# Optimization experiments

Measured on AMD Instinct MI355X. Metric: run time of the kernel, lower is better.

## Reference

```python
import jax, jax.numpy as jnp
import numpy as np

N = 50000      # nodes
E = 800000     # edges
IN = 128       # input features (arxiv)
HID = 128      # hidden per head
HEADS = 3      # arxiv_data=True -> 3 heads
OUT = 40       # classes
EPS = 1e-5     # BN eps
SLOPE = 0.2    # DGL GATConv leaky_relu negative slope


def setup_inputs() -> dict:
    key = jax.random.key(0)
    ks = jax.random.split(key, 20)
    x = jax.random.normal(ks[0], (N, IN), jnp.float32)
    src = jax.random.randint(ks[1], (E,), 0, N, dtype=jnp.int32)
    # guarantee every node has >=1 in-edge so edge_softmax is well-defined
    dst = jnp.concatenate([jnp.arange(N, dtype=jnp.int32),
                           jax.random.randint(ks[2], (E - N,), 0, N, dtype=jnp.int32)])

    def lin(k, fi, fo):
        return jax.random.normal(k, (fi, fo), jnp.float32) * (1.0 / np.sqrt(fi))

    def attn(k, h, d):
        return jax.random.normal(k, (h, d), jnp.float32) * 0.1

    return {
        "x": x, "src": src, "dst": dst,
        # layer 0: IN -> HEADS*HID
        "W0": lin(ks[3], IN, HEADS * HID),
        "al0": attn(ks[4], HEADS, HID), "ar0": attn(ks[5], HEADS, HID),
        "b0": jnp.zeros((HEADS * HID,), jnp.float32),
        # layer 1: HEADS*HID -> HEADS*HID
        "W1": lin(ks[6], HEADS * HID, HEADS * HID),
        "al1": attn(ks[7], HEADS, HID), "ar1": attn(ks[8], HEADS, HID),
        "b1": jnp.zeros((HEADS * HID,), jnp.float32),
        # layer 2: HEADS*HID -> OUT, 1 head
        "W2": lin(ks[9], HEADS * HID, OUT),
        "al2": attn(ks[10], 1, OUT), "ar2": attn(ks[11], 1, OUT),
        "b2": jnp.zeros((OUT,), jnp.float32),
        # batch norms over HEADS*HID channels
        "g0": jnp.ones((HEADS * HID,), jnp.float32), "be0": jnp.zeros((HEADS * HID,), jnp.float32),
        "g1": jnp.ones((HEADS * HID,), jnp.float32), "be1": jnp.zeros((HEADS * HID,), jnp.float32),
    }


def gat_layer(h, src, dst, W, al, ar, b, heads, d_out):
    # fc + per-head split: [N, heads, d_out]
    f = (h @ W).reshape(-1, heads, d_out)
    el = jnp.einsum('nhd,hd->nh', f, al)          # [N, H]
    er = jnp.einsum('nhd,hd->nh', f, ar)          # [N, H]
    e = jax.nn.leaky_relu(el[src] + er[dst], SLOPE)  # [E, H]
    # edge softmax over incoming edges of each dst node
    m = jax.ops.segment_max(e, dst, num_segments=N)
    ex = jnp.exp(e - m[dst])
    s = jax.ops.segment_sum(ex, dst, num_segments=N)
    a = ex / s[dst]                                # [E, H]
    # u_mul_e + sum aggregation
    out = jax.ops.segment_sum(f[src] * a[:, :, None], dst, num_segments=N)  # [N, H, D]
    out = out + b.reshape(1, heads, d_out)
    return out.reshape(-1, heads * d_out)


def batch_norm(h, g, b):
    mu = h.mean(axis=0)
    var = h.var(axis=0)
    return g * (h - mu) / jnp.sqrt(var + EPS) + b


def reference(x, src, dst, W0, al0, ar0, b0, W1, al1, ar1, b1,
              W2, al2, ar2, b2, g0, be0, g1, be1):
    h = gat_layer(x, src, dst, W0, al0, ar0, b0, HEADS, HID)
    h = jax.nn.relu(batch_norm(h, g0, be0))        # dropout: eval mode (identity)
    h = gat_layer(h, src, dst, W1, al1, ar1, b1, HEADS, HID)
    h = jax.nn.relu(batch_norm(h, g1, be1))
    out = gat_layer(h, src, dst, W2, al2, ar2, b2, 1, OUT)
    return out
```

## Files before the change

kernel.cpp:

```cpp
#include <hip/hip_runtime.h>
#include <hip/hip_bf16.h>

typedef __hip_bfloat16 bf16;
typedef __attribute__((ext_vector_type(8))) short short8;
typedef __attribute__((ext_vector_type(4))) float f32x4;

static constexpr int N_NODES  = 50000;
static constexpr int N_EDGES  = 800000;
static constexpr int F_IN     = 128;
static constexpr int D_HID    = 128;
static constexpr int H_HEADS  = 3;
static constexpr int F_OUT    = 40;
static constexpr float BN_EPS = 1e-5f;
static constexpr float SLOPE  = 0.2f;

__device__ __forceinline__ float bfLo(unsigned int u) { return __uint_as_float(u << 16); }
__device__ __forceinline__ float bfHi(unsigned int u) { return __uint_as_float(u & 0xffff0000u); }
__device__ __forceinline__ float bfs(unsigned short s) { return __uint_as_float(((unsigned int)s) << 16); }
__device__ __forceinline__ unsigned int packbf(float a, float b) {
  union { bf16 h[2]; unsigned int u; } pk;
  pk.h[0] = __float2bfloat16(a);
  pk.h[1] = __float2bfloat16(b);
  return pk.u;
}
__device__ __forceinline__ short f2bf_s(float v) {
  bf16 h = __float2bfloat16(v);
  union { bf16 b; short s; } c; c.b = h; return c.s;
}

__global__ __launch_bounds__(256) void gemm_mfma(const short* __restrict__ A,
                                                 const short* __restrict__ WT,
                                                 bf16* __restrict__ C,
                                                 const float* __restrict__ alp,
                                                 const float* __restrict__ arp,
                                                 float* __restrict__ el,
                                                 float* __restrict__ er,
                                                 const float* __restrict__ scale,
                                                 const float* __restrict__ shift,
                                                 int M, int K, int Nc, int els, int ers,
                                                 int lda, int adiag) {
  constexpr int BM = 128, BN = 128, BK = 64, LDP = BK + 8;
  __shared__ short As[BM * LDP];
  __shared__ short Bs[BN * LDP];
  __shared__ float ecomb[128][4];
  int tid = threadIdx.x;
  int wave = tid >> 6, lane = tid & 63;
  int bm = blockIdx.y, bn = blockIdx.x;
  int m15 = lane & 15, quad = lane >> 4;
  int ksub = quad * 8;
  int wr = wave >> 1, wc = wave & 1;
  int srow = tid >> 3;
  int scol = (tid & 7) * 8;
  int acol0 = adiag ? bn * K : 0;

  f32x4 acc[4][4];
#pragma unroll
  for (int i = 0; i < 4; ++i)
#pragma unroll
    for (int j = 0; j < 4; ++j) acc[i][j] = (f32x4){0.f, 0.f, 0.f, 0.f};

  for (int k0 = 0; k0 < K; k0 += BK) {
    int cb = acol0 + k0 + scol;
    f32x4 sc0, sc1, sh0, sh1;
    if (scale) {
      sc0 = *(const f32x4*)&scale[cb]; sc1 = *(const f32x4*)&scale[cb + 4];
      sh0 = *(const f32x4*)&shift[cb]; sh1 = *(const f32x4*)&shift[cb + 4];
    }
#pragma unroll
    for (int c = 0; c < 4; ++c) {
      int r = srow + c * 32;
      int gr = bm * BM + r; if (gr >= M) gr = M - 1;
      short8 av = *(const short8*)&A[(size_t)gr * lda + acol0 + k0 + scol];
      if (scale) {
#pragma unroll
        for (int j = 0; j < 8; ++j) {
          float v = bfs((unsigned short)av[j]);
          float s = (j < 4) ? ((const float*)&sc0)[j] : ((const float*)&sc1)[j - 4];
          float t = (j < 4) ? ((const float*)&sh0)[j] : ((const float*)&sh1)[j - 4];
          float y = v * s + t;
          av[j] = f2bf_s(y > 0.f ? y : 0.f);
        }
      }
      *(short8*)&As[r * LDP + scol] = av;
      int gn = bn * BN + r;
      *(short8*)&Bs[r * LDP + scol] = *(const short8*)&WT[(size_t)gn * K + k0 + scol];
    }
    __syncthreads();
#pragma unroll
    for (int ks = 0; ks < BK; ks += 32) {
      short8 a[4], b[4];
#pragma unroll
      for (int i = 0; i < 4; ++i)
        a[i] = *(const short8*)&As[(wr * 64 + i * 16 + m15) * LDP + ks + ksub];
#pragma unroll
      for (int j = 0; j < 4; ++j)
        b[j] = *(const short8*)&Bs[(wc * 64 + j * 16 + m15) * LDP + ks + ksub];
#pragma unroll
      for (int i = 0; i < 4; ++i)
#pragma unroll
        for (int j = 0; j < 4; ++j)
          acc[i][j] = __builtin_amdgcn_mfma_f32_16x16x32_bf16(a[i], b[j], acc[i][j], 0, 0, 0);
    }
    __syncthreads();
  }

  int h = bn;
  float alv[4], arv[4];
#pragma unroll
  for (int j = 0; j < 4; ++j) {
    int col = bn * BN + wc * 64 + j * 16 + m15;
    alv[j] = alp[col];
    arv[j] = arp[col];
  }
#pragma unroll
  for (int i = 0; i < 4; ++i) {
#pragma unroll
    for (int r = 0; r < 4; ++r) {
      int rl = wr * 64 + i * 16 + quad * 4 + r;
      int row = bm * BM + rl;
      float pe = 0.f, pr = 0.f;
#pragma unroll
      for (int j = 0; j < 4; ++j) {
        float v = acc[i][j][r];
        pe += v * alv[j];
        pr += v * arv[j];
        int col = bn * BN + wc * 64 + j * 16 + m15;
        if (row < M && col < Nc)
          C[(size_t)row * Nc + col] = __float2bfloat16(v);
      }
#pragma unroll
      for (int off = 1; off < 16; off <<= 1) {
        pe += __shfl_xor(pe, off);
        pr += __shfl_xor(pr, off);
      }
      if (m15 == 0) {
        ecomb[rl][wc] = pe;
        ecomb[rl][2 + wc] = pr;
      }
    }
  }
  __syncthreads();
  if (tid < 128) {
    int row = bm * BM + tid;
    if (row < M) {
      el[(size_t)row * els + h] = ecomb[tid][0] + ecomb[tid][1];
      er[(size_t)row * ers + h] = ecomb[tid][2] + ecomb[tid][3];
    }
  }
}

__global__ void prep_kernel(const float* __restrict__ x, bf16* __restrict__ abuf,
                            const float* __restrict__ W0, const float* __restrict__ W1,
                            const float* __restrict__ W2, bf16* __restrict__ WT0,
                            bf16* __restrict__ WT1, bf16* __restrict__ WT2,
                            const float* __restrict__ al2, const float* __restrict__ ar2,
                            float* __restrict__ alp2, float* __restrict__ arp2,
                            int* __restrict__ cnt) {
  const int NTOT = N_NODES * F_IN;
  for (int i = blockIdx.x * blockDim.x + threadIdx.x; i < NTOT;
       i += gridDim.x * blockDim.x) {
    abuf[i] = __float2bfloat16(x[i]);
    if (i < 384 * 384) { int n = i / 384, k = i - n * 384; WT1[i] = __float2bfloat16(W1[(size_t)k * 384 + n]); }
    if (i < 384 * 128) { int n = i / 128, k = i - n * 128; WT0[i] = __float2bfloat16(W0[(size_t)k * 384 + n]); }
    if (i < 128 * 384) { int n = i / 384, k = i - n * 384; WT2[i] = __float2bfloat16(n < F_OUT ? W2[(size_t)k * F_OUT + n] : 0.f); }
    if (i < 2 * N_NODES) cnt[i] = 0;
    if (i < 128) { alp2[i] = i < F_OUT ? al2[i] : 0.f; arp2[i] = i < F_OUT ? ar2[i] : 0.f; }
  }
}

__global__ __launch_bounds__(256) void vlr_kernel(const float* __restrict__ W0,
                                                  const float* __restrict__ al0,
                                                  const float* __restrict__ ar0,
                                                  float* __restrict__ vl,
                                                  float* __restrict__ vr) {
  int wid = (blockIdx.x * 256 + threadIdx.x) >> 6;
  int lane = threadIdx.x & 63;
  int h = wid >> 7, k = wid & 127;
  const float2* wrow = (const float2*)(W0 + (size_t)k * 384 + h * 128);
  const float2* av = (const float2*)(al0 + h * 128);
  const float2* rv = (const float2*)(ar0 + h * 128);
  float2 wv = wrow[lane], a2 = av[lane], r2 = rv[lane];
  float sl = wv.x * a2.x + wv.y * a2.y;
  float sr = wv.x * r2.x + wv.y * r2.y;
#pragma unroll
  for (int off = 32; off > 0; off >>= 1) {
    sl += __shfl_xor(sl, off);
    sr += __shfl_xor(sr, off);
  }
  if (lane == 0) { vl[wid] = sl; vr[wid] = sr; }
}

__global__ __launch_bounds__(256) void elr_kernel(const unsigned int* __restrict__ x2,
                                                  const float* __restrict__ vl,
                                                  const float* __restrict__ vr,
                                                  float* __restrict__ el,
                                                  float* __restrict__ er, int N) {
  int wv = threadIdx.x >> 6, lane = threadIdx.x & 63;
  int n = blockIdx.x * 4 + wv;
  if (n >= N) return;
  unsigned int u = x2[(size_t)n * 64 + lane];
  float v0 = bfLo(u), v1 = bfHi(u);
  float pl[3], pr[3];
#pragma unroll
  for (int h = 0; h < 3; ++h) {
    float2 a2 = *(const float2*)&vl[h * 128 + 2 * lane];
    float2 r2 = *(const float2*)&vr[h * 128 + 2 * lane];
    pl[h] = v0 * a2.x + v1 * a2.y;
    pr[h] = v0 * r2.x + v1 * r2.y;
  }
#pragma unroll
  for (int h = 0; h < 3; ++h) {
#pragma unroll
    for (int off = 32; off > 0; off >>= 1) {
      pl[h] += __shfl_xor(pl[h], off);
      pr[h] += __shfl_xor(pr[h], off);
    }
  }
  if (lane == 0) {
    *(float4*)&el[(size_t)n * 4] = make_float4(pl[0], pl[1], pl[2], 0.f);
    er[(size_t)n * 3 + 0] = pr[0];
    er[(size_t)n * 3 + 1] = pr[1];
    er[(size_t)n * 3 + 2] = pr[2];
  }
}

__global__ void hist_kernel(const int* __restrict__ dst, int* __restrict__ cnt, int E) {
  int i = blockIdx.x * blockDim.x + threadIdx.x;
  if (i < E) atomicAdd(cnt + dst[i], 1);
}

__global__ void scan_part_kernel(const int* __restrict__ cnt, int* __restrict__ blksum, int N) {
  __shared__ int sh[256];
  int i = blockIdx.x * 256 + threadIdx.x;
  sh[threadIdx.x] = (i < N) ? cnt[i] : 0;
  __syncthreads();
  for (int off = 128; off > 0; off >>= 1) {
    if (threadIdx.x < off) sh[threadIdx.x] += sh[threadIdx.x + off];
    __syncthreads();
  }
  if (threadIdx.x == 0) blksum[blockIdx.x] = sh[0];
}

__global__ void scan_write_kernel(const int* __restrict__ cnt, const int* __restrict__ blksum,
                                  int* __restrict__ row_ptr, int N, int E, int nblk) {
  __shared__ int top[256];
  __shared__ int sh[256];
  int t = threadIdx.x;
  int vt = (t < nblk) ? blksum[t] : 0;
  top[t] = vt;
  __syncthreads();
  for (int off = 1; off < 256; off <<= 1) {
    int u = (t >= off) ? top[t - off] : 0;
    __syncthreads();
    top[t] += u;
    __syncthreads();
  }
  int blkoff = (blockIdx.x == 0) ? 0 : top[blockIdx.x - 1];
  int i = blockIdx.x * 256 + t;
  int v = (i < N) ? cnt[i] : 0;
  sh[t] = v;
  __syncthreads();
  for (int off = 1; off < 256; off <<= 1) {
    int u = (t >= off) ? sh[t - off] : 0;
    __syncthreads();
    sh[t] += u;
    __syncthreads();
  }
  if (i < N) row_ptr[i] = blkoff + sh[t] - v;
  if (i == 0) row_ptr[N] = E;
}

__global__ void scatter_kernel(const int* __restrict__ src, const int* __restrict__ dst,
                               const int* __restrict__ row_ptr, int* __restrict__ fill,
                               int* __restrict__ csr_src, int E) {
  int i = blockIdx.x * blockDim.x + threadIdx.x;
  if (i < E) {
    int d = dst[i];
    int pos = row_ptr[d] + atomicAdd(fill + d, 1);
    csr_src[pos] = src[i];
  }
}

__global__ __launch_bounds__(256) void aggr_x_kernel(
    const int* __restrict__ row_ptr, const int* __restrict__ csr_src,
    const float4* __restrict__ el4, const float* __restrict__ er,
    const uint4* __restrict__ xq, uint4* __restrict__ outq,
    float* __restrict__ bnzero, int N) {
  if (blockIdx.x == 0) {
    for (int j = threadIdx.x; j < 2 * H_HEADS * D_HID; j += 256) bnzero[j] = 0.f;
  }
  __shared__ float wls[4][64 * 3];
  __shared__ int   sls[4][64];
  int wv = threadIdx.x >> 6;
  int d = (blockIdx.x * 256 + threadIdx.x) >> 6;
  int lane = threadIdx.x & 63;
  if (d >= N) return;
  int beg = row_ptr[d], end = row_ptr[d + 1];
  float* mywls = wls[wv];
  int* mysls = sls[wv];
  int g = lane >> 4;
  int cch = lane & 15;

  float erd[3];
#pragma unroll
  for (int h = 0; h < 3; ++h) erd[h] = er[d * 3 + h];
  float acc[3][8];
#pragma unroll
  for (int h = 0; h < 3; ++h)
#pragma unroll
    for (int j = 0; j < 8; ++j) acc[h][j] = 0.f;
  float sp[3] = {0.f, 0.f, 0.f};

  for (int k0 = beg; k0 < end; k0 += 64) {
    int nk = end - k0; if (nk > 64) nk = 64;
    if (lane < nk) {
      int s_l = csr_src[k0 + lane];
      mysls[lane] = s_l;
      float4 e4 = el4[s_l];
      float ev[3] = {e4.x, e4.y, e4.z};
#pragma unroll
      for (int h = 0; h < 3; ++h) {
        float sc = ev[h] + erd[h];
        sc = sc > 0.f ? sc : SLOPE * sc;
        float w = __expf(sc);
        mywls[lane * 3 + h] = w;
        sp[h] += w;
      }
    }
    for (int e0 = 0; e0 < nk; e0 += 4) {
      int e = e0 + g;
      if (e < nk) {
        int se = mysls[e];
        float w0s = mywls[e * 3], w1s = mywls[e * 3 + 1], w2s = mywls[e * 3 + 2];
        uint4 u = xq[(size_t)se * 16 + cch];
        float ff[8] = {bfLo(u.x), bfHi(u.x), bfLo(u.y), bfHi(u.y),
                       bfLo(u.z), bfHi(u.z), bfLo(u.w), bfHi(u.w)};
#pragma unroll
        for (int j = 0; j < 8; ++j) {
          acc[0][j] += w0s * ff[j];
          acc[1][j] += w1s * ff[j];
          acc[2][j] += w2s * ff[j];
        }
      }
    }
  }
#pragma unroll
  for (int h = 0; h < 3; ++h) {
#pragma unroll
    for (int off = 32; off > 0; off >>= 1) sp[h] += __shfl_xor(sp[h], off);
  }
#pragma unroll
  for (int h = 0; h < 3; ++h)
#pragma unroll
    for (int j = 0; j < 8; ++j) {
      acc[h][j] += __shfl_xor(acc[h][j], 16);
      acc[h][j] += __shfl_xor(acc[h][j], 32);
    }
  if (g < 3) {
    float og[8];
#pragma unroll
    for (int j = 0; j < 8; ++j)
      og[j] = (g == 0) ? acc[0][j] : (g == 1) ? acc[1][j] : acc[2][j];
    float spg = (g == 0) ? sp[0] : (g == 1) ? sp[1] : sp[2];
    float inv = 1.f / spg;
    uint4 r;
    r.x = packbf(og[0] * inv, og[1] * inv);
    r.y = packbf(og[2] * inv, og[3] * inv);
    r.z = packbf(og[4] * inv, og[5] * inv);
    r.w = packbf(og[6] * inv, og[7] * inv);
    outq[(size_t)d * 48 + g * 16 + cch] = r;
  }
}

template <int H, int D>
__global__ __launch_bounds__(256) void aggr_fused_kernel(
    const int* __restrict__ row_ptr, const int* __restrict__ csr_src,
    const float4* __restrict__ el4, const float* __restrict__ er,
    const bf16* __restrict__ f, uint4* __restrict__ outq,
    float* __restrict__ bnzero, int N) {
  if (blockIdx.x == 0) {
    for (int j = threadIdx.x; j < 2 * H * D; j += 256) bnzero[j] = 0.f;
  }
  constexpr int W = H * D / 2;
  constexpr int WQ = W / 4;
  __shared__ float wls[4][64 * H];
  int wv = threadIdx.x >> 6;
  int d = (blockIdx.x * 256 + threadIdx.x) >> 6;
  int lane = threadIdx.x & 63;
  if (d >= N) return;
  int beg = row_ptr[d], end = row_ptr[d + 1];
  const uint4* fq = (const uint4*)f;
  float* mywls = wls[wv];
  int hsel = lane >> 4;

  float erd[H];
#pragma unroll
  for (int h = 0; h < H; ++h) erd[h] = er[d * H + h];
  float acc[8];
#pragma unroll
  for (int j = 0; j < 8; ++j) acc[j] = 0.f;
  float sp[H];
#pragma unroll
  for (int h = 0; h < H; ++h) sp[h] = 0.f;

  for (int k0 = beg; k0 < end; k0 += 64) {
    int nk = end - k0; if (nk > 64) nk = 64;
    int s_l = 0;
    if (lane < nk) {
      s_l = csr_src[k0 + lane];
      float4 e4 = el4[s_l];
      float ev[3] = {e4.x, e4.y, e4.z};
#pragma unroll
      for (int h = 0; h < H; ++h) {
        float sc = ev[h] + erd[h];
        sc = sc > 0.f ? sc : SLOPE * sc;
        float w = __expf(sc);
        mywls[lane * H + h] = w;
        sp[h] += w;
      }
    }
    for (int e = 0; e < nk; ++e) {
      int se = __shfl(s_l, e);
      if (lane < WQ) {
        float w = mywls[e * H + hsel];
        uint4 u = fq[(size_t)se * WQ + lane];
        acc[0] += w * bfLo(u.x); acc[1] += w * bfHi(u.x);
        acc[2] += w * bfLo(u.y); acc[3] += w * bfHi(u.y);
        acc[4] += w * bfLo(u.z); acc[5] += w * bfHi(u.z);
        acc[6] += w * bfLo(u.w); acc[7] += w * bfHi(u.w);
      }
    }
  }
#pragma unroll
  for (int h = 0; h < H; ++h) {
#pragma unroll
    for (int off = 32; off > 0; off >>= 1) sp[h] += __shfl_xor(sp[h], off);
  }
  if (lane < WQ) {
    float inv = 1.f / sp[hsel];
    uint4 r;
    r.x = packbf(acc[0] * inv, acc[1] * inv);
    r.y = packbf(acc[2] * inv, acc[3] * inv);
    r.z = packbf(acc[4] * inv, acc[5] * inv);
    r.w = packbf(acc[6] * inv, acc[7] * inv);
    outq[(size_t)d * WQ + lane] = r;
  }
}

__global__ __launch_bounds__(256) void aggr_out_kernel(
    const int* __restrict__ row_ptr, const int* __restrict__ csr_src,
    const float* __restrict__ el, const float* __restrict__ er,
    const bf16* __restrict__ f, const float* __restrict__ bias,
    float* __restrict__ out, int N) {
  constexpr int DW = F_OUT / 2;
  __shared__ float wls[4][64];
  __shared__ int   sls[4][64];
  int wv = threadIdx.x >> 6;
  int d = (blockIdx.x * 256 + threadIdx.x) >> 6;
  int lane = threadIdx.x & 63;
  if (d >= N) return;
  int beg = row_ptr[d], end = row_ptr[d + 1];
  const unsigned int* fu = (const unsigned int*)f;
  float* mywls = wls[wv];
  int* mysls = sls[wv];
  int g = lane / DW;
  int cch = lane - g * DW;
  float erd = er[d];
  float a0 = 0.f, a1 = 0.f, sp = 0.f;
  for (int k0 = beg; k0 < end; k0 += 64) {
    int nk = end - k0; if (nk > 64) nk = 64;
    if (lane < nk) {
      int s_l = csr_src[k0 + lane];
      mysls[lane] = s_l;
      float sc = el[s_l] + erd;
      sc = sc > 0.f ? sc : SLOPE * sc;
      float w = __expf(sc);
      mywls[lane] = w;
      sp += w;
    }
    for (int e0 = 0; e0 < nk; e0 += 3) {
      int e = e0 + g;
      if (g < 3 && e < nk) {
        int se = mysls[e];
        float w = mywls[e];
        unsigned int u = fu[(size_t)se * DW + cch];
        a0 += w * bfLo(u);
        a1 += w * bfHi(u);
      }
    }
  }
#pragma unroll
  for (int off = 32; off > 0; off >>= 1) sp += __shfl_xor(sp, off);
  float b0 = __shfl(a0, (lane + DW) & 63), b1 = __shfl(a1, (lane + DW) & 63);
  float c0 = __shfl(a0, (lane + 2 * DW) & 63), c1 = __shfl(a1, (lane + 2 * DW) & 63);
  if (lane < DW) {
    float inv = 1.f / sp;
    float o0 = (a0 + b0 + c0) * inv + bias[2 * lane];
    float o1 = (a1 + b1 + c1) * inv + bias[2 * lane + 1];
    *(float2*)&out[(size_t)d * F_OUT + 2 * lane] = make_float2(o0, o1);
  }
}

__global__ void bn_stats_kernel(const unsigned int* __restrict__ h2, float* __restrict__ sum,
                                float* __restrict__ sumsq, int N, int C2) {
  int c = threadIdx.x;
  int step = gridDim.x;
  float s0 = 0.f, q0 = 0.f, s1 = 0.f, q1 = 0.f;
  int n = blockIdx.x;
  for (; n + 3 * step < N; n += 4 * step) {
    unsigned int ua = h2[(size_t)n * C2 + c];
    unsigned int ub = h2[(size_t)(n + step) * C2 + c];
    unsigned int uc = h2[(size_t)(n + 2 * step) * C2 + c];
    unsigned int ud = h2[(size_t)(n + 3 * step) * C2 + c];
    float va0 = bfLo(ua), va1 = bfHi(ua);
    float vb0 = bfLo(ub), vb1 = bfHi(ub);
    float vc0 = bfLo(uc), vc1 = bfHi(uc);
    float vd0 = bfLo(ud), vd1 = bfHi(ud);
    s0 += va0 + vb0 + vc0 + vd0;
    s1 += va1 + vb1 + vc1 + vd1;
    q0 += va0 * va0 + vb0 * vb0 + vc0 * vc0 + vd0 * vd0;
    q1 += va1 * va1 + vb1 * vb1 + vc1 * vc1 + vd1 * vd1;
  }
  for (; n < N; n += step) {
    unsigned int u = h2[(size_t)n * C2 + c];
    float v0 = bfLo(u), v1 = bfHi(u);
    s0 += v0; q0 += v0 * v0;
    s1 += v1; q1 += v1 * v1;
  }
  atomicAdd(sum + 2 * c, s0);
  atomicAdd(sum + 2 * c + 1, s1);
  atomicAdd(sumsq + 2 * c, q0);
  atomicAdd(sumsq + 2 * c + 1, q1);
}

__global__ void bn_finalize_kernel(const float* __restrict__ sum, const float* __restrict__ sumsq,
                                   const float* __restrict__ g, const float* __restrict__ be,
                                   float* __restrict__ scale, float* __restrict__ shift,
                                   int N, int C) {
  int c = threadIdx.x;
  if (c >= C) return;
  float inv_n = 1.f / (float)N;
  float mu = sum[c] * inv_n;
  float var = sumsq[c] * inv_n - mu * mu;
  float sc = g[c] * rsqrtf(var + BN_EPS);
  scale[c] = sc;
  shift[c] = be[c] - mu * sc;
}

static inline int cdiv(int a, int b) { return (a + b - 1) / b; }

extern "C" void kernel_launch(void* const* d_in, const int* in_sizes, int n_in,
                              void* d_out, int out_size, void* d_ws, size_t ws_size,
                              hipStream_t stream) {
  const float* x   = (const float*)d_in[0];
  const int* src   = (const int*)d_in[1];
  const int* dst   = (const int*)d_in[2];
  const float* W0  = (const float*)d_in[3];
  const float* al0 = (const float*)d_in[4];
  const float* ar0 = (const float*)d_in[5];
  const float* W1  = (const float*)d_in[7];
  const float* al1 = (const float*)d_in[8];
  const float* ar1 = (const float*)d_in[9];
  const float* W2  = (const float*)d_in[11];
  const float* al2 = (const float*)d_in[12];
  const float* ar2 = (const float*)d_in[13];
  const float* b2  = (const float*)d_in[14];
  const float* g0  = (const float*)d_in[15];
  const float* be0 = (const float*)d_in[16];
  const float* g1  = (const float*)d_in[17];
  const float* be1 = (const float*)d_in[18];
  float* out = (float*)d_out;

  const int N = N_NODES, E = N_EDGES, H = H_HEADS;
  const int C = H * D_HID;
  const int nblk = cdiv(N, 256);

  char* p = (char*)d_ws;
  auto take = [&](size_t bytes) {
    char* r = p;
    p += (bytes + 255) & ~(size_t)255;
    return r;
  };
  bf16*   f_buf   = (bf16*) take((size_t)N * C * sizeof(bf16));
  bf16*   hbuf    = (bf16*) take((size_t)N * C * sizeof(bf16));
  bf16*   abuf    = (bf16*) take((size_t)N * C * sizeof(bf16));
  float*  elbuf   = (float*)take((size_t)N * 4 * sizeof(float));
  float*  er      = (float*)take((size_t)N * H * sizeof(float));
  float*  bnbuf   = (float*)take((size_t)2 * C * sizeof(float));
  float*  scbuf   = (float*)take((size_t)2 * C * sizeof(float));
  bf16*   WT0     = (bf16*) take((size_t)C * F_IN * sizeof(bf16));
  bf16*   WT1     = (bf16*) take((size_t)C * C * sizeof(bf16));
  bf16*   WT2     = (bf16*) take((size_t)128 * C * sizeof(bf16));
  float*  alp2    = (float*)take(128 * sizeof(float));
  float*  arp2    = (float*)take(128 * sizeof(float));
  float*  vlbuf   = (float*)take(384 * sizeof(float));
  float*  vrbuf   = (float*)take(384 * sizeof(float));
  int*    cnt     = (int*)take((size_t)2 * N * sizeof(int));
  int*    row_ptr = (int*)take((size_t)(N + 1) * sizeof(int));
  int*    csr_src = (int*)take((size_t)E * sizeof(int));
  int*    blksum  = (int*)take(256 * sizeof(int));
  float*  bnsum = bnbuf, *bnsq = bnbuf + C;
  float*  scv = scbuf, *shv = scbuf + C;
  int*    fill  = cnt + N;

  prep_kernel<<<cdiv(N * F_IN, 256), 256, 0, stream>>>(x, abuf, W0, W1, W2, WT0, WT1, WT2,
                                                       al2, ar2, alp2, arp2, cnt);
  vlr_kernel<<<96, 256, 0, stream>>>(W0, al0, ar0, vlbuf, vrbuf);
  elr_kernel<<<cdiv(N, 4), 256, 0, stream>>>((const unsigned int*)abuf, vlbuf, vrbuf,
                                             elbuf, er, N);
  hist_kernel<<<cdiv(E, 256), 256, 0, stream>>>(dst, cnt, E);
  scan_part_kernel<<<nblk, 256, 0, stream>>>(cnt, blksum, N);
  scan_write_kernel<<<nblk, 256, 0, stream>>>(cnt, blksum, row_ptr, N, E, nblk);
  scatter_kernel<<<cdiv(E, 256), 256, 0, stream>>>(src, dst, row_ptr, fill, csr_src, E);

  aggr_x_kernel<<<cdiv(N * 64, 256), 256, 0, stream>>>(
      row_ptr, csr_src, (const float4*)elbuf, er, (const uint4*)abuf,
      (uint4*)f_buf, bnbuf, N);
  gemm_mfma<<<dim3(3, cdiv(N, 128)), 256, 0, stream>>>(
      (const short*)f_buf, (const short*)WT0, hbuf, al0, ar0, elbuf, er,
      nullptr, nullptr, N, F_IN, C, 4, 3, C, 1);
  bn_stats_kernel<<<1024, C / 2, 0, stream>>>((const unsigned int*)hbuf, bnsum, bnsq, N, C / 2);
  bn_finalize_kernel<<<1, C, 0, stream>>>(bnsum, bnsq, g0, be0, scv, shv, N, C);

  gemm_mfma<<<dim3(C / 128, cdiv(N, 128)), 256, 0, stream>>>(
      (const short*)hbuf, (const short*)WT1, f_buf, al1, ar1, elbuf, er,
      scv, shv, N, C, C, 4, 3, C, 0);
  aggr_fused_kernel<H_HEADS, D_HID><<<cdiv(N * 64, 256), 256, 0, stream>>>(
      row_ptr, csr_src, (const float4*)elbuf, er, f_buf, (uint4*)hbuf, bnbuf, N);
  bn_stats_kernel<<<1024, C / 2, 0, stream>>>((const unsigned int*)hbuf, bnsum, bnsq, N, C / 2);
  bn_finalize_kernel<<<1, C, 0, stream>>>(bnsum, bnsq, g1, be1, scv, shv, N, C);

  gemm_mfma<<<dim3(1, cdiv(N, 128)), 256, 0, stream>>>(
      (const short*)hbuf, (const short*)WT2, f_buf, alp2, arp2, elbuf, er,
      scv, shv, N, C, F_OUT, 1, 1, C, 0);
  aggr_out_kernel<<<cdiv(N * 64, 256), 256, 0, stream>>>(
      row_ptr, csr_src, elbuf, er, f_buf, b2, out, N);
}
```

Measured before the change: 598.7 us.

## Process four edges per wavefront iteration in fused GAT aggregation

Restructures the per-node aggregation so each 16-lane group handles a different edge, with each lane loading three 16-byte chunks (one per head), instead of only 48 of 64 lanes working on one edge at a time. Partial sums are combined across the four lane groups with cross-lane shuffles at the end. The aim is to use all lanes, keep more loads in flight and cut the serial edge loop length by four. The cost is more accumulator registers (24 floats) and an extra cross-lane reduction per node. The head count is now hardcoded to 3 instead of following the template parameter.

```diff
diff --git a/kernel.cpp b/kernel.cpp
--- a/kernel.cpp
+++ b/kernel.cpp
@@ -381,9 +381,9 @@
   if (blockIdx.x == 0) {
     for (int j = threadIdx.x; j < 2 * H * D; j += 256) bnzero[j] = 0.f;
   }
-  constexpr int W = H * D / 2;
-  constexpr int WQ = W / 4;
-  __shared__ float wls[4][64 * H];
+  constexpr int WQ = H * D / 8;
+  __shared__ float wls[4][64 * 3];
+  __shared__ int   sls[4][64];
   int wv = threadIdx.x >> 6;
   int d = (blockIdx.x * 256 + threadIdx.x) >> 6;
   int lane = threadIdx.x & 63;
@@ -391,59 +391,85 @@
   int beg = row_ptr[d], end = row_ptr[d + 1];
   const uint4* fq = (const uint4*)f;
   float* mywls = wls[wv];
-  int hsel = lane >> 4;
-
-  float erd[H];
-#pragma unroll
-  for (int h = 0; h < H; ++h) erd[h] = er[d * H + h];
-  float acc[8];
-#pragma unroll
-  for (int j = 0; j < 8; ++j) acc[j] = 0.f;
-  float sp[H];
-#pragma unroll
-  for (int h = 0; h < H; ++h) sp[h] = 0.f;
+  int* mysls = sls[wv];
+  int g = lane >> 4;
+  int cch = lane & 15;
+
+  float erd[3];
+#pragma unroll
+  for (int h = 0; h < 3; ++h) erd[h] = er[d * 3 + h];
+  float acc[3][8];
+#pragma unroll
+  for (int p = 0; p < 3; ++p)
+#pragma unroll
+    for (int j = 0; j < 8; ++j) acc[p][j] = 0.f;
+  float sp[3] = {0.f, 0.f, 0.f};
 
   for (int k0 = beg; k0 < end; k0 += 64) {
     int nk = end - k0; if (nk > 64) nk = 64;
-    int s_l = 0;
     if (lane < nk) {
-      s_l = csr_src[k0 + lane];
+      int s_l = csr_src[k0 + lane];
+      mysls[lane] = s_l;
       float4 e4 = el4[s_l];
       float ev[3] = {e4.x, e4.y, e4.z};
 #pragma unroll
-      for (int h = 0; h < H; ++h) {
+      for (int h = 0; h < 3; ++h) {
         float sc = ev[h] + erd[h];
         sc = sc > 0.f ? sc : SLOPE * sc;
         float w = __expf(sc);
-        mywls[lane * H + h] = w;
+        mywls[lane * 3 + h] = w;
         sp[h] += w;
       }
     }
-    for (int e = 0; e < nk; ++e) {
-      int se = __shfl(s_l, e);
-      if (lane < WQ) {
-        float w = mywls[e * H + hsel];
-        uint4 u = fq[(size_t)se * WQ + lane];
-        acc[0] += w * bfLo(u.x); acc[1] += w * bfHi(u.x);
-        acc[2] += w * bfLo(u.y); acc[3] += w * bfHi(u.y);
-        acc[4] += w * bfLo(u.z); acc[5] += w * bfHi(u.z);
-        acc[6] += w * bfLo(u.w); acc[7] += w * bfHi(u.w);
-      }
-    }
-  }
-#pragma unroll
-  for (int h = 0; h < H; ++h) {
+    for (int e0 = 0; e0 < nk; e0 += 4) {
+      int e = e0 + g;
+      if (e < nk) {
+        int se = mysls[e];
+        float w0s = mywls[e * 3], w1s = mywls[e * 3 + 1], w2s = mywls[e * 3 + 2];
+        const uint4* rp = &fq[(size_t)se * WQ + cch];
+        uint4 u0 = rp[0];
+        uint4 u1 = rp[16];
+        uint4 u2 = rp[32];
+        acc[0][0] += w0s * bfLo(u0.x); acc[0][1] += w0s * bfHi(u0.x);
+        acc[0][2] += w0s * bfLo(u0.y); acc[0][3] += w0s * bfHi(u0.y);
+        acc[0][4] += w0s * bfLo(u0.z); acc[0][5] += w0s * bfHi(u0.z);
+        acc[0][6] += w0s * bfLo(u0.w); acc[0][7] += w0s * bfHi(u0.w);
+        acc[1][0] += w1s * bfLo(u1.x); acc[1][1] += w1s * bfHi(u1.x);
+        acc[1][2] += w1s * bfLo(u1.y); acc[1][3] += w1s * bfHi(u1.y);
+        acc[1][4] += w1s * bfLo(u1.z); acc[1][5] += w1s * bfHi(u1.z);
+        acc[1][6] += w1s * bfLo(u1.w); acc[1][7] += w1s * bfHi(u1.w);
+        acc[2][0] += w2s * bfLo(u2.x); acc[2][1] += w2s * bfHi(u2.x);
+        acc[2][2] += w2s * bfLo(u2.y); acc[2][3] += w2s * bfHi(u2.y);
+        acc[2][4] += w2s * bfLo(u2.z); acc[2][5] += w2s * bfHi(u2.z);
+        acc[2][6] += w2s * bfLo(u2.w); acc[2][7] += w2s * bfHi(u2.w);
+      }
+    }
+  }
+#pragma unroll
+  for (int h = 0; h < 3; ++h) {
 #pragma unroll
     for (int off = 32; off > 0; off >>= 1) sp[h] += __shfl_xor(sp[h], off);
   }
-  if (lane < WQ) {
-    float inv = 1.f / sp[hsel];
+#pragma unroll
+  for (int p = 0; p < 3; ++p)
+#pragma unroll
+    for (int j = 0; j < 8; ++j) {
+      acc[p][j] += __shfl_xor(acc[p][j], 16);
+      acc[p][j] += __shfl_xor(acc[p][j], 32);
+    }
+  if (g < 3) {
+    float og[8];
+#pragma unroll
+    for (int j = 0; j < 8; ++j)
+      og[j] = (g == 0) ? acc[0][j] : (g == 1) ? acc[1][j] : acc[2][j];
+    float spg = (g == 0) ? sp[0] : (g == 1) ? sp[1] : sp[2];
+    float inv = 1.f / spg;
     uint4 r;
-    r.x = packbf(acc[0] * inv, acc[1] * inv);
-    r.y = packbf(acc[2] * inv, acc[3] * inv);
-    r.z = packbf(acc[4] * inv, acc[5] * inv);
-    r.w = packbf(acc[6] * inv, acc[7] * inv);
-    outq[(size_t)d * WQ + lane] = r;
+    r.x = packbf(og[0] * inv, og[1] * inv);
+    r.y = packbf(og[2] * inv, og[3] * inv);
+    r.z = packbf(og[4] * inv, og[5] * inv);
+    r.w = packbf(og[6] * inv, og[7] * inv);
+    outq[(size_t)d * WQ + g * 16 + cch] = r;
   }
 }
 
```

Measured after the change: 606.4 us. Within noise of the previous version (+1.3%).

## Fuse BN stats into layer-0 GEMM epilogue and merge small setup kernels

Applied to the files above, without the earlier changes.

Layer-0 batch-norm sum and sum-of-squares are now accumulated in the GEMM epilogue with per-column atomics, which removes one bn_stats pass over hbuf. The vl/vr projection is folded into prep_kernel and the dst histogram into elr_kernel, cutting two launches. The final GEMM output now uses a padded 64-column row stride for better-aligned gathers in aggr_out. The changes add atomic contention on BN columns and give float sums a nondeterministic order. They also assume bnbuf is zero, since the bn_stats kernel that presumably reset it no longer runs for layer 0.

```diff
diff --git a/kernel.cpp b/kernel.cpp
--- a/kernel.cpp
+++ b/kernel.cpp
@@ -37,8 +37,9 @@
                                                  float* __restrict__ er,
                                                  const float* __restrict__ scale,
                                                  const float* __restrict__ shift,
+                                                 float* __restrict__ bnstats,
                                                  int M, int K, int Nc, int els, int ers,
-                                                 int lda, int adiag) {
+                                                 int lda, int ldc, int adiag) {
   constexpr int BM = 128, BN = 128, BK = 64, LDP = BK + 8;
   __shared__ short As[BM * LDP];
   __shared__ short Bs[BN * LDP];
@@ -112,6 +113,7 @@
     alv[j] = alp[col];
     arv[j] = arp[col];
   }
+  float csum[4] = {0.f, 0.f, 0.f, 0.f}, csq[4] = {0.f, 0.f, 0.f, 0.f};
 #pragma unroll
   for (int i = 0; i < 4; ++i) {
 #pragma unroll
@@ -124,9 +126,10 @@
         float v = acc[i][j][r];
         pe += v * alv[j];
         pr += v * arv[j];
+        if (bnstats && row < M) { csum[j] += v; csq[j] += v * v; }
         int col = bn * BN + wc * 64 + j * 16 + m15;
         if (row < M && col < Nc)
-          C[(size_t)row * Nc + col] = __float2bfloat16(v);
+          C[(size_t)row * ldc + col] = __float2bfloat16(v);
       }
 #pragma unroll
       for (int off = 1; off < 16; off <<= 1) {
@@ -136,6 +139,21 @@
       if (m15 == 0) {
         ecomb[rl][wc] = pe;
         ecomb[rl][2 + wc] = pr;
+      }
+    }
+  }
+  if (bnstats) {
+#pragma unroll
+    for (int j = 0; j < 4; ++j) {
+      csum[j] += __shfl_xor(csum[j], 16); csum[j] += __shfl_xor(csum[j], 32);
+      csq[j]  += __shfl_xor(csq[j], 16);  csq[j]  += __shfl_xor(csq[j], 32);
+    }
+    if (quad == 0) {
+#pragma unroll
+      for (int j = 0; j < 4; ++j) {
+        int col = bn * BN + wc * 64 + j * 16 + m15;
+        atomicAdd(bnstats + col, csum[j]);
+        atomicAdd(bnstats + Nc + col, csq[j]);
       }
     }
   }
@@ -155,7 +173,9 @@
                             bf16* __restrict__ WT1, bf16* __restrict__ WT2,
                             const float* __restrict__ al2, const float* __restrict__ ar2,
                             float* __restrict__ alp2, float* __restrict__ arp2,
-                            int* __restrict__ cnt) {
+                            int* __restrict__ cnt,
+                            const float* __restrict__ al0, const float* __restrict__ ar0,
+                            float* __restrict__ vl, float* __restrict__ vr) {
   const int NTOT = N_NODES * F_IN;
   for (int i = blockIdx.x * blockDim.x + threadIdx.x; i < NTOT;
        i += gridDim.x * blockDim.x) {
@@ -166,35 +186,35 @@
     if (i < 2 * N_NODES) cnt[i] = 0;
     if (i < 128) { alp2[i] = i < F_OUT ? al2[i] : 0.f; arp2[i] = i < F_OUT ? ar2[i] : 0.f; }
   }
-}
-
-__global__ __launch_bounds__(256) void vlr_kernel(const float* __restrict__ W0,
-                                                  const float* __restrict__ al0,
-                                                  const float* __restrict__ ar0,
-                                                  float* __restrict__ vl,
-                                                  float* __restrict__ vr) {
-  int wid = (blockIdx.x * 256 + threadIdx.x) >> 6;
-  int lane = threadIdx.x & 63;
-  int h = wid >> 7, k = wid & 127;
-  const float2* wrow = (const float2*)(W0 + (size_t)k * 384 + h * 128);
-  const float2* av = (const float2*)(al0 + h * 128);
-  const float2* rv = (const float2*)(ar0 + h * 128);
-  float2 wv = wrow[lane], a2 = av[lane], r2 = rv[lane];
-  float sl = wv.x * a2.x + wv.y * a2.y;
-  float sr = wv.x * r2.x + wv.y * r2.y;
-#pragma unroll
-  for (int off = 32; off > 0; off >>= 1) {
-    sl += __shfl_xor(sl, off);
-    sr += __shfl_xor(sr, off);
-  }
-  if (lane == 0) { vl[wid] = sl; vr[wid] = sr; }
+  if (blockIdx.x < 96) {
+    int wid = blockIdx.x * 4 + (threadIdx.x >> 6);
+    int lane = threadIdx.x & 63;
+    int h = wid >> 7, k = wid & 127;
+    const float2* wrow = (const float2*)(W0 + (size_t)k * 384 + h * 128);
+    const float2* av = (const float2*)(al0 + h * 128);
+    const float2* rv = (const float2*)(ar0 + h * 128);
+    float2 wv = wrow[lane], a2 = av[lane], r2 = rv[lane];
+    float sl = wv.x * a2.x + wv.y * a2.y;
+    float sr = wv.x * r2.x + wv.y * r2.y;
+#pragma unroll
+    for (int off = 32; off > 0; off >>= 1) {
+      sl += __shfl_xor(sl, off);
+      sr += __shfl_xor(sr, off);
+    }
+    if (lane == 0) { vl[wid] = sl; vr[wid] = sr; }
+  }
 }
 
 __global__ __launch_bounds__(256) void elr_kernel(const unsigned int* __restrict__ x2,
                                                   const float* __restrict__ vl,
                                                   const float* __restrict__ vr,
                                                   float* __restrict__ el,
-                                                  float* __restrict__ er, int N) {
+                                                  float* __restrict__ er,
+                                                  const int* __restrict__ dst,
+                                                  int* __restrict__ cnt,
+                                                  int N, int E) {
+  int gid = blockIdx.x * 256 + threadIdx.x;
+  if (gid < E) atomicAdd(cnt + dst[gid], 1);
   int wv = threadIdx.x >> 6, lane = threadIdx.x & 63;
   int n = blockIdx.x * 4 + wv;
   if (n >= N) return;
@@ -222,11 +242,6 @@
     er[(size_t)n * 3 + 1] = pr[1];
     er[(size_t)n * 3 + 2] = pr[2];
   }
-}
-
-__global__ void hist_kernel(const int* __restrict__ dst, int* __restrict__ cnt, int E) {
-  int i = blockIdx.x * blockDim.x + threadIdx.x;
-  if (i < E) atomicAdd(cnt + dst[i], 1);
 }
 
 __global__ void scan_part_kernel(const int* __restrict__ cnt, int* __restrict__ blksum, int N) {
@@ -453,6 +468,7 @@
     const bf16* __restrict__ f, const float* __restrict__ bias,
     float* __restrict__ out, int N) {
   constexpr int DW = F_OUT / 2;
+  constexpr int LDW = 32;
   __shared__ float wls[4][64];
   __shared__ int   sls[4][64];
   int wv = threadIdx.x >> 6;
@@ -483,7 +499,7 @@
       if (g < 3 && e < nk) {
         int se = mysls[e];
         float w = mywls[e];
-        unsigned int u = fu[(size_t)se * DW + cch];
+        unsigned int u = fu[(size_t)se * LDW + cch];
         a0 += w * bfLo(u);
         a1 += w * bfHi(u);
       }
@@ -604,11 +620,10 @@
   int*    fill  = cnt + N;
 
   prep_kernel<<<cdiv(N * F_IN, 256), 256, 0, stream>>>(x, abuf, W0, W1, W2, WT0, WT1, WT2,
-                                                       al2, ar2, alp2, arp2, cnt);
-  vlr_kernel<<<96, 256, 0, stream>>>(W0, al0, ar0, vlbuf, vrbuf);
+                                                       al2, ar2, alp2, arp2, cnt,
+                                                       al0, ar0, vlbuf, vrbuf);
   elr_kernel<<<cdiv(N, 4), 256, 0, stream>>>((const unsigned int*)abuf, vlbuf, vrbuf,
-                                             elbuf, er, N);
-  hist_kernel<<<cdiv(E, 256), 256, 0, stream>>>(dst, cnt, E);
+                                             elbuf, er, dst, cnt, N, E);
   scan_part_kernel<<<nblk, 256, 0, stream>>>(cnt, blksum, N);
   scan_write_kernel<<<nblk, 256, 0, stream>>>(cnt, blksum, row_ptr, N, E, nblk);
   scatter_kernel<<<cdiv(E, 256), 256, 0, stream>>>(src, dst, row_ptr, fill, csr_src, E);
@@ -618,13 +633,12 @@
       (uint4*)f_buf, bnbuf, N);
   gemm_mfma<<<dim3(3, cdiv(N, 128)), 256, 0, stream>>>(
       (const short*)f_buf, (const short*)WT0, hbuf, al0, ar0, elbuf, er,
-      nullptr, nullptr, N, F_IN, C, 4, 3, C, 1);
-  bn_stats_kernel<<<1024, C / 2, 0, stream>>>((const unsigned int*)hbuf, bnsum, bnsq, N, C / 2);
+      nullptr, nullptr, bnbuf, N, F_IN, C, 4, 3, C, C, 1);
   bn_finalize_kernel<<<1, C, 0, stream>>>(bnsum, bnsq, g0, be0, scv, shv, N, C);
 
   gemm_mfma<<<dim3(C / 128, cdiv(N, 128)), 256, 0, stream>>>(
       (const short*)hbuf, (const short*)WT1, f_buf, al1, ar1, elbuf, er,
-      scv, shv, N, C, C, 4, 3, C, 0);
+      scv, shv, nullptr, N, C, C, 4, 3, C, C, 0);
   aggr_fused_kernel<H_HEADS, D_HID><<<cdiv(N * 64, 256), 256, 0, stream>>>(
       row_ptr, csr_src, (const float4*)elbuf, er, f_buf, (uint4*)hbuf, bnbuf, N);
   bn_stats_kernel<<<1024, C / 2, 0, stream>>>((const unsigned int*)hbuf, bnsum, bnsq, N, C / 2);
@@ -632,7 +646,7 @@
 
   gemm_mfma<<<dim3(1, cdiv(N, 128)), 256, 0, stream>>>(
       (const short*)hbuf, (const short*)WT2, f_buf, alp2, arp2, elbuf, er,
-      scv, shv, N, C, F_OUT, 1, 1, C, 0);
+      scv, shv, nullptr, N, C, F_OUT, 1, 1, C, 64, 0);
   aggr_out_kernel<<<cdiv(N * 64, 256), 256, 0, stream>>>(
       row_ptr, csr_src, elbuf, er, f_buf, b2, out, N);
 }
```

Result: faster. 554.7 us (-7.3%).
